# Optimization experiments

Measured on AMD Instinct MI355X. Metric: run time of the kernel, lower is better.

The kernel has to match this reference:

```python
import jax, jax.numpy as jnp
import numpy as np

B, N, H = 32, 1024, 512
THR = 0.05  # peak_detection_threshold


def _l2norm(x):
    return x / jnp.linalg.norm(x, axis=-1, keepdims=True)


def setup_inputs() -> dict:
    key = jax.random.key(0)
    ks = jax.random.split(key, 6)
    def w(k, shape, fan_in):
        return jax.random.normal(k, shape, jnp.float32) / np.float32(np.sqrt(fan_in))
    return {
        "segment_rep": jax.random.normal(ks[0], (B, N, H), jnp.float32),
        "phn_mask": jnp.ones((B, N), jnp.float32),
        # SegmentSimilarityMeasure: Linear(2H->H), ReLU, Linear(H->1, no bias)
        "W1": w(ks[1], (2 * H, H), 2 * H),
        "b1": jnp.zeros((H,), jnp.float32),
        "W2": w(ks[2], (H, 1), H),
        # word_enc: Linear(H->H), ReLU, Linear(H->H)
        "We1": w(ks[3], (H, H), H),
        "be1": jnp.zeros((H,), jnp.float32),
        "We2": w(ks[4], (H, H), H),
        "be2": jnp.zeros((H,), jnp.float32),
    }


def _forward(segment_rep, phn_mask, W1, b1, W2, We1, be1, We2, be2):
    Bs, Np, Hd = segment_rep.shape
    # adjacent segment similarity: MLP on concat of l2-normalized neighbors -> (B, N-1)
    cat = jnp.concatenate([_l2norm(segment_rep[:, :-1, :]), _l2norm(segment_rep[:, 1:, :])], axis=2)
    S = (jax.nn.relu(cat @ W1 + b1) @ W2)[..., 0]

    # relative dissimilarity
    Smin = jnp.min(S, axis=1, keepdims=True)
    Smax = jnp.max(S, axis=1, keepdims=True)
    D = 1.0 - (S - Smin) / (Smax - Smin)

    # peak detector (faithful to original, incl. final overwrite of first-order cols -2:)
    z = jnp.zeros_like(D)
    fo = z
    fo = fo.at[:, 0].set(jnp.maximum(D[:, 0] - D[:, 1], 0.0))
    fo = fo.at[:, 1:-1].set(jnp.minimum(jnp.maximum(D[:, 1:-1] - D[:, :-2], 0.0),
                                        jnp.maximum(D[:, 1:-1] - D[:, 2:], 0.0)))
    fo = fo.at[:, -1].set(jnp.maximum(D[:, -1] - D[:, -2], 0.0))
    so = z
    so = so.at[:, 0:2].set(jnp.maximum(D[:, 0:2] - D[:, 2:4], 0.0))
    so = so.at[:, 2:-2].set(jnp.minimum(jnp.maximum(D[:, 2:-2] - D[:, :-4], 0.0),
                                        jnp.maximum(D[:, 2:-2] - D[:, 4:], 0.0)))
    fo = fo.at[:, -2:].set(jnp.maximum(D[:, -2:] - D[:, -4:-2], 0.0))  # replicates original code
    P = jnp.minimum(jnp.maximum(jnp.maximum(fo, so) - THR, 0.0), fo)

    # pad, mask, straight-through hard boundaries
    P = jnp.pad(P, ((0, 0), (0, 1)))
    P = jax.nn.relu(P + (phn_mask - 1.0))
    b_soft = jnp.tanh(10.0 * P)
    b_hard = jnp.tanh(100000.0 * P)
    b = b_soft + jax.lax.stop_gradient(b_hard - b_soft)
    b = jnp.cumsum(b, axis=1)  # (B, N)
    b = b + (b[:, :1] == 0).astype(b.dtype)  # per-row +1 if b[:,0]==0
    num_word_segments = b[:, -1].astype(jnp.int32) + 1  # (B,)

    # U: column j holds j+1 for j < num_word_segments[i], else -100000. Nmax = N (static bound).
    cols = jnp.arange(1, Np + 1, dtype=jnp.int32)  # (Nmax,)
    U = jnp.where(cols[None, :] <= num_word_segments[:, None],
                  cols.astype(segment_rep.dtype)[None, :], -100000.0)  # (B, Nmax)

    V = U[:, None, :] - b[:, :, None]  # (B, N, Nmax)
    Wseg = 1.0 - jnp.tanh(100000.0 * jnp.abs(V))
    Wseg = Wseg / jnp.sum(Wseg, axis=1, keepdims=True)
    Wseg = jnp.nan_to_num(Wseg)

    # pool: (B, Nmax, N) @ (B, N, H) -> (B, Nmax, H)
    word_rep = jnp.einsum('bnm,bnh->bmh', Wseg, segment_rep)
    word_masks = jnp.where(word_rep == 0, 0.0, 1.0)
    out = jax.nn.relu(word_rep @ We1 + be1) @ We2 + be2
    return out * word_masks


def reference(segment_rep, phn_mask, W1, b1, W2, We1, be1, We2, be2):
    return _forward(segment_rep, phn_mask, W1, b1, W2, We1, be1, We2, be2)
```

## Files before the change

### kernel.cpp

```cpp
#include <hip/hip_runtime.h>

#define BB 32
#define NN 1024
#define HH 512
#define NS 1023

typedef unsigned short u16;
typedef unsigned int   u32;
typedef __attribute__((ext_vector_type(8))) short bf16x8;
typedef __attribute__((ext_vector_type(4))) float f32x4;

__device__ __forceinline__ float bf2f(u16 h) {
  union { u32 u; float f; } c; c.u = ((u32)h) << 16; return c.f;
}
__device__ __forceinline__ u16 f2bf(float f) {
  union { float f; u32 u; } c; c.f = f;
  u32 u = c.u;
  return (u16)((u + 0x7fffu + ((u >> 16) & 1u)) >> 16);
}
__device__ __forceinline__ void split_bf(float x, u16& hi, u16& lo) {
  hi = f2bf(x);
  lo = f2bf(x - bf2f(hi));
}
__device__ __forceinline__ void dma16(const u16* g, u16* l) {
  __builtin_amdgcn_global_load_lds(
      (const __attribute__((address_space(1))) u32*)g,
      (__attribute__((address_space(3))) u32*)l, 16, 0, 0);
}

__global__ __launch_bounds__(256) void k_prep_a(const float* __restrict__ seg,
                                                u16* __restrict__ ahi,
                                                u16* __restrict__ alo) {
  int row = blockIdx.x * 4 + (threadIdx.x >> 6);
  int lane = threadIdx.x & 63;
  const float4* p = (const float4*)(seg + ((size_t)row << 9) + lane * 8);
  float4 a = p[0], b = p[1];
  float v[8] = {a.x, a.y, a.z, a.w, b.x, b.y, b.z, b.w};
  float s = 0.f;
#pragma unroll
  for (int i = 0; i < 8; ++i) s += v[i] * v[i];
#pragma unroll
  for (int m = 32; m; m >>= 1) s += __shfl_xor(s, m, 64);
  float nrm = sqrtf(s);
  u16 h[8], l[8];
#pragma unroll
  for (int i = 0; i < 8; ++i) split_bf(v[i] / nrm, h[i], l[i]);
  size_t off = ((size_t)row << 9) + lane * 8;
  *(uint4*)(ahi + off) = make_uint4(h[0] | (h[1] << 16), h[2] | (h[3] << 16),
                                    h[4] | (h[5] << 16), h[6] | (h[7] << 16));
  *(uint4*)(alo + off) = make_uint4(l[0] | (l[1] << 16), l[2] | (l[3] << 16),
                                    l[4] | (l[5] << 16), l[6] | (l[7] << 16));
}

__global__ __launch_bounds__(256) void k_tr3(const float* __restrict__ W1,
                                             const float* __restrict__ We1,
                                             const float* __restrict__ We2,
                                             u16* __restrict__ w1h,
                                             u16* __restrict__ w1l,
                                             u16* __restrict__ we1t,
                                             u16* __restrict__ we2t) {
  __shared__ u16 Th[64 * 66], Tl[64 * 66];
  int z = blockIdx.z;
  const float* src; u16 *dh, *dl; int K, N;
  if (z == 0)      { src = W1;  dh = w1h;  dl = w1l;          K = 1024; N = 512; }
  else if (z == 1) { src = We1; dh = we1t; dl = (u16*)0;      K = 512;  N = 512; }
  else             { src = We2; dh = we2t; dl = (u16*)0;      K = 512;  N = 512; }
  if (blockIdx.y * 64 >= K) return;
  int nb = blockIdx.x * 64, kb = blockIdx.y * 64;
  int tid = threadIdx.x;
#pragma unroll
  for (int i = 0; i < 16; ++i) {
    int e = tid + i * 256;
    int r = e >> 6, c = e & 63;
    float v = src[(size_t)(kb + r) * N + nb + c];
    u16 hi, lo; split_bf(v, hi, lo);
    Th[c * 66 + r] = hi;
    Tl[c * 66 + r] = lo;
  }
  __syncthreads();
#pragma unroll
  for (int i = 0; i < 16; ++i) {
    int e = tid + i * 256;
    int n = e >> 6, k = e & 63;
    dh[(size_t)(nb + n) * K + kb + k] = Th[n * 66 + k];
    if (dl) dl[(size_t)(nb + n) * K + kb + k] = Tl[n * 66 + k];
  }
}

__global__ __launch_bounds__(512, 2) void k_sgemm(const u16* __restrict__ ahi,
                                                  const u16* __restrict__ alo,
                                                  const u16* __restrict__ w1h,
                                                  const u16* __restrict__ w1l,
                                                  const float* __restrict__ b1,
                                                  const float* __restrict__ W2,
                                                  float* __restrict__ Spart) {
  __shared__ u16 Ah[2][256 * 32];
  __shared__ u16 Al[2][256 * 32];
  __shared__ u16 Bh[2][256 * 32];
  __shared__ u16 Bl[2][256 * 32];

  const int tid  = threadIdx.x;
  const int wave = tid >> 6, lane = tid & 63;
  const int quad = lane >> 4, l15 = lane & 15;
  const int wm = wave >> 2, wn = wave & 3;
  const int r_in = lane >> 2, c_in = lane & 3;
  const int w    = blockIdx.x;
  const int xcd  = w & 7, slot = w >> 3;
  const int nblk = slot & 1;
  const int mblk = xcd * 16 + (slot >> 1);
  const int mrow0 = mblk * 256;
  const int ncol0 = nblk * 256;

#define SG_AH(tb_, ks_)                                                      \
  {                                                                          \
    int k0_ = (ks_) * 32, half_ = k0_ >> 9, cb_ = k0_ & 511;                 \
    int g0_ = mrow0 + wave * 32 + r_in + half_;                              \
    int g1_ = g0_ + 16;                                                      \
    if (g0_ > 32767) g0_ = 32767;                                            \
    if (g1_ > 32767) g1_ = 32767;                                            \
    dma16(ahi + ((((size_t)g0_) << 9) + cb_ + c_in * 8),                     \
          &Ah[tb_][(wave * 32) * 32]);                                       \
    dma16(ahi + ((((size_t)g1_) << 9) + cb_ + c_in * 8),                     \
          &Ah[tb_][(wave * 32 + 16) * 32]);                                  \
  }
#define SG_AL(tb_, ks_)                                                      \
  {                                                                          \
    int k0_ = (ks_) * 32, half_ = k0_ >> 9, cb_ = k0_ & 511;                 \
    int g0_ = mrow0 + wave * 32 + r_in + half_;                              \
    int g1_ = g0_ + 16;                                                      \
    if (g0_ > 32767) g0_ = 32767;                                            \
    if (g1_ > 32767) g1_ = 32767;                                            \
    dma16(alo + ((((size_t)g0_) << 9) + cb_ + c_in * 8),                     \
          &Al[tb_][(wave * 32) * 32]);                                       \
    dma16(alo + ((((size_t)g1_) << 9) + cb_ + c_in * 8),                     \
          &Al[tb_][(wave * 32 + 16) * 32]);                                  \
  }
#define SG_BH(tb_, ks_)                                                      \
  {                                                                          \
    int k0_ = (ks_) * 32;                                                    \
    int n0_ = ncol0 + wave * 32 + r_in;                                      \
    dma16(w1h + (((size_t)n0_) << 10) + k0_ + c_in * 8,                      \
          &Bh[tb_][(wave * 32) * 32]);                                       \
    dma16(w1h + (((size_t)(n0_ + 16)) << 10) + k0_ + c_in * 8,               \
          &Bh[tb_][(wave * 32 + 16) * 32]);                                  \
  }
#define SG_BL(tb_, ks_)                                                      \
  {                                                                          \
    int k0_ = (ks_) * 32;                                                    \
    int n0_ = ncol0 + wave * 32 + r_in;                                      \
    dma16(w1l + (((size_t)n0_) << 10) + k0_ + c_in * 8,                      \
          &Bl[tb_][(wave * 32) * 32]);                                       \
    dma16(w1l + (((size_t)(n0_ + 16)) << 10) + k0_ + c_in * 8,               \
          &Bl[tb_][(wave * 32 + 16) * 32]);                                  \
  }

  f32x4 acc[8][4];
#pragma unroll
  for (int mi = 0; mi < 8; ++mi)
#pragma unroll
    for (int ni = 0; ni < 4; ++ni) acc[mi][ni] = (f32x4){0.f, 0.f, 0.f, 0.f};

  SG_AH(0, 0) SG_BH(0, 0) SG_BL(0, 0) SG_AL(0, 0)
  __syncthreads();

  for (int ks = 0; ks < 32; ++ks) {
    const int bb = ks & 1;
    const int nx = (ks + 1 < 32) ? ks + 1 : 31;

    SG_AH(bb ^ 1, nx) SG_BH(bb ^ 1, nx) SG_BL(bb ^ 1, nx) SG_AL(bb ^ 1, nx)

    bf16x8 ah[8], al[8], bh[4], bl[4];
#pragma unroll
    for (int mi = 0; mi < 8; ++mi)
      ah[mi] = *(const bf16x8*)&Ah[bb][(wm * 128 + mi * 16 + l15) * 32 + quad * 8];
#pragma unroll
    for (int ni = 0; ni < 4; ++ni)
      bh[ni] = *(const bf16x8*)&Bh[bb][(wn * 64 + ni * 16 + l15) * 32 + quad * 8];
    __builtin_amdgcn_s_setprio(1);
#pragma unroll
    for (int ni = 0; ni < 4; ++ni)
#pragma unroll
      for (int mi = 0; mi < 8; ++mi)
        acc[mi][ni] = __builtin_amdgcn_mfma_f32_16x16x32_bf16(ah[mi], bh[ni], acc[mi][ni], 0, 0, 0);
#pragma unroll
    for (int ni = 0; ni < 4; ++ni)
      bl[ni] = *(const bf16x8*)&Bl[bb][(wn * 64 + ni * 16 + l15) * 32 + quad * 8];
#pragma unroll
    for (int ni = 0; ni < 4; ++ni)
#pragma unroll
      for (int mi = 0; mi < 8; ++mi)
        acc[mi][ni] = __builtin_amdgcn_mfma_f32_16x16x32_bf16(ah[mi], bl[ni], acc[mi][ni], 0, 0, 0);
#pragma unroll
    for (int mi = 0; mi < 8; ++mi)
      al[mi] = *(const bf16x8*)&Al[bb][(wm * 128 + mi * 16 + l15) * 32 + quad * 8];
#pragma unroll
    for (int ni = 0; ni < 4; ++ni)
#pragma unroll
      for (int mi = 0; mi < 8; ++mi)
        acc[mi][ni] = __builtin_amdgcn_mfma_f32_16x16x32_bf16(al[mi], bh[ni], acc[mi][ni], 0, 0, 0);
    __builtin_amdgcn_s_setprio(0);

    __syncthreads();
  }
#undef SG_AH
#undef SG_AL
#undef SG_BH
#undef SG_BL

  float* red = (float*)&Ah[0][0];
  float b1v[4], w2v[4];
#pragma unroll
  for (int ni = 0; ni < 4; ++ni) {
    int n_g = ncol0 + wn * 64 + ni * 16 + l15;
    b1v[ni] = b1[n_g];
    w2v[ni] = W2[n_g];
  }
#pragma unroll
  for (int mi = 0; mi < 8; ++mi) {
#pragma unroll
    for (int reg = 0; reg < 4; ++reg) {
      float part = 0.f;
#pragma unroll
      for (int ni = 0; ni < 4; ++ni) {
        float h = acc[mi][ni][reg] + b1v[ni];
        h = h > 0.f ? h : 0.f;
        part = fmaf(h, w2v[ni], part);
      }
#pragma unroll
      for (int m = 8; m; m >>= 1) part += __shfl_xor(part, m, 64);
      if (l15 == 0) red[wave * 128 + mi * 16 + quad * 4 + reg] = part;
    }
  }
  __syncthreads();
  if (tid < 256) {
    int wmr = tid >> 7, rl = tid & 127;
    float s = red[(wmr * 4 + 0) * 128 + rl] + red[(wmr * 4 + 1) * 128 + rl]
            + red[(wmr * 4 + 2) * 128 + rl] + red[(wmr * 4 + 3) * 128 + rl];
    int grow = mrow0 + tid;
    int b = grow >> 10, n = grow & 1023;
    if (n < NS)
      Spart[((size_t)nblk * BB + b) * NN + n] = s;
  }
}

__global__ __launch_bounds__(256) void k_row(const float* __restrict__ S0,
                                             const float* __restrict__ S1,
                                             const float* __restrict__ mask,
                                             int* __restrict__ assign,
                                             float* __restrict__ weight,
                                             float* __restrict__ total,
                                             int* __restrict__ startn,
                                             int* __restrict__ endn) {
  int b = blockIdx.x, tid = threadIdx.x;
  __shared__ float Ssh[NS];
  __shared__ float Dsh[NS];
  __shared__ float tsh[NN];
  __shared__ float bsh[NN];
  __shared__ float totl[NN];
  __shared__ int   stl[NN];
  __shared__ int   enl[NN];
  __shared__ float red[256];

  for (int n = tid; n < NS; n += 256)
    Ssh[n] = S0[((size_t)b << 10) + n] + S1[((size_t)b << 10) + n];
  __syncthreads();

  float mn = INFINITY, mx = -INFINITY;
  for (int n = tid; n < NS; n += 256) {
    float v = Ssh[n];
    mn = fminf(mn, v); mx = fmaxf(mx, v);
  }
  red[tid] = mn; __syncthreads();
  for (int s = 128; s; s >>= 1) { if (tid < s) red[tid] = fminf(red[tid], red[tid + s]); __syncthreads(); }
  float Smin = red[0]; __syncthreads();
  red[tid] = mx; __syncthreads();
  for (int s = 128; s; s >>= 1) { if (tid < s) red[tid] = fmaxf(red[tid], red[tid + s]); __syncthreads(); }
  float Smax = red[0]; __syncthreads();

  for (int n = tid; n < NS; n += 256)
    Dsh[n] = 1.0f - (Ssh[n] - Smin) / (Smax - Smin);
  __syncthreads();

  for (int n = tid; n < NN; n += 256) {
    float P;
    if (n >= NS) {
      P = 0.f;
    } else {
      float D = Dsh[n];
      float fo, so;
      if (n == 0)            fo = fmaxf(D - Dsh[1], 0.f);
      else if (n >= NS - 2)  fo = fmaxf(D - Dsh[n - 2], 0.f);
      else                   fo = fminf(fmaxf(D - Dsh[n - 1], 0.f),
                                        fmaxf(D - Dsh[n + 1], 0.f));
      if (n <= 1)            so = fmaxf(D - Dsh[n + 2], 0.f);
      else if (n >= NS - 2)  so = 0.f;
      else                   so = fminf(fmaxf(D - Dsh[n - 2], 0.f),
                                        fmaxf(D - Dsh[n + 2], 0.f));
      P = fminf(fmaxf(fmaxf(fo, so) - 0.05f, 0.f), fo);
    }
    float m = mask[((size_t)b << 10) + n];
    P = P + (m - 1.0f);
    P = P > 0.f ? P : 0.f;
    float bs = tanhf(10.0f * P);
    float bh = tanhf(100000.0f * P);
    tsh[n] = bs + (bh - bs);
  }
  __syncthreads();

  if (tid == 0) {
    float acc = 0.f;
    for (int n = 0; n < NN; n += 8) {
      float t0 = tsh[n + 0], t1 = tsh[n + 1], t2 = tsh[n + 2], t3 = tsh[n + 3];
      float t4 = tsh[n + 4], t5 = tsh[n + 5], t6 = tsh[n + 6], t7 = tsh[n + 7];
      acc += t0; bsh[n + 0] = acc; acc += t1; bsh[n + 1] = acc;
      acc += t2; bsh[n + 2] = acc; acc += t3; bsh[n + 3] = acc;
      acc += t4; bsh[n + 4] = acc; acc += t5; bsh[n + 5] = acc;
      acc += t6; bsh[n + 6] = acc; acc += t7; bsh[n + 7] = acc;
    }
  }
  __syncthreads();

  float add1 = (bsh[0] == 0.0f) ? 1.0f : 0.0f;
  int   num  = (int)(bsh[NN - 1] + add1) + 1;

  for (int mi = tid; mi < NN; mi += 256) { totl[mi] = 0.f; stl[mi] = 1 << 30; enl[mi] = -1; }
  __syncthreads();

  for (int n = tid; n < NN; n += 256) {
    float bv = bsh[n] + add1;
    float kf = rintf(bv);
    int   k  = (int)kf;
    int   a  = -1; float w = 0.f;
    if (k >= 1 && k <= num && k <= NN) {
      float v = fabsf(kf - bv);
      w = 1.0f - tanhf(100000.0f * v);
      if (w > 0.f) {
        a = k - 1;
        atomicAdd(&totl[a], w);
        atomicMin(&stl[a], n);
        atomicMax(&enl[a], n);
      } else {
        a = -1; w = 0.f;
      }
    }
    assign[((size_t)b << 10) + n] = a;
    weight[((size_t)b << 10) + n] = w;
  }
  __syncthreads();
  for (int mi = tid; mi < NN; mi += 256) {
    total [((size_t)b << 10) + mi] = totl[mi];
    startn[((size_t)b << 10) + mi] = stl[mi];
    endn  [((size_t)b << 10) + mi] = enl[mi];
  }
}

__global__ __launch_bounds__(64) void k_pool(const float* __restrict__ seg,
                                             const int* __restrict__ assign,
                                             const float* __restrict__ weight,
                                             const float* __restrict__ total,
                                             const int* __restrict__ startn,
                                             const int* __restrict__ endn,
                                             u16* hrep,
                                             unsigned char* __restrict__ mb) {
  int bm = blockIdx.x;
  int b  = bm >> 10, m = bm & 1023;
  int lane = threadIdx.x;
  float acc[8] = {0.f, 0.f, 0.f, 0.f, 0.f, 0.f, 0.f, 0.f};
  float tm = total[bm];
  if (tm > 0.f) {
    int s = startn[bm], e = endn[bm];
    for (int n = s; n <= e; ++n) {
      if (assign[((size_t)b << 10) + n] != m) continue;
      float coef = weight[((size_t)b << 10) + n] / tm;
      const float4* p = (const float4*)(seg + (((size_t)b << 10) + n) * HH + lane * 8);
      float4 x = p[0], y = p[1];
      acc[0] = fmaf(coef, x.x, acc[0]); acc[1] = fmaf(coef, x.y, acc[1]);
      acc[2] = fmaf(coef, x.z, acc[2]); acc[3] = fmaf(coef, x.w, acc[3]);
      acc[4] = fmaf(coef, y.x, acc[4]); acc[5] = fmaf(coef, y.y, acc[5]);
      acc[6] = fmaf(coef, y.z, acc[6]); acc[7] = fmaf(coef, y.w, acc[7]);
    }
  }
  u16 h[8];
  unsigned int mbyte = 0;
#pragma unroll
  for (int j = 0; j < 8; ++j) {
    h[j] = f2bf(acc[j]);
    mbyte |= (acc[j] == 0.f ? 1u : 0u) << j;
  }
  *(uint4*)(hrep + ((size_t)bm << 10) + lane * 8) =
      make_uint4(h[0] | (h[1] << 16), h[2] | (h[3] << 16),
                 h[4] | (h[5] << 16), h[6] | (h[7] << 16));
  mb[((size_t)bm << 6) + lane] = (unsigned char)mbyte;
}

__global__ __launch_bounds__(512, 4) void k_g(const u16* asrc,
                                              const u16* __restrict__ bmat,
                                              const float* __restrict__ bias,
                                              const unsigned char* __restrict__ mb,
                                              float* outp,
                                              u16* hid,
                                              int a_off, int mode) {
  __shared__ u16 As[3][64 * 32];
  __shared__ u16 Bs[2][512 * 32];

  const int tid  = threadIdx.x;
  const int wave = tid >> 6, lane = tid & 63;
  const int quad = lane >> 4, l15 = lane & 15;
  const int wm = wave >> 2, wn = wave & 3;
  const int r_in = lane >> 2, c_in = lane & 3;
  const int mrow0 = blockIdx.x * 64;

#define SGB(tb_, ks_)                                                        \
  {                                                                          \
    int k0_ = (ks_) * 32;                                                    \
    _Pragma("unroll")                                                        \
    for (int g_ = 0; g_ < 4; ++g_) {                                         \
      int n_ = wave * 64 + g_ * 16 + r_in;                                   \
      dma16(bmat + (size_t)n_ * 512 + k0_ + c_in * 8,                        \
            &Bs[tb_][(wave * 64 + g_ * 16) * 32]);                           \
    }                                                                        \
  }
#define SGA(sl_, ks_)                                                        \
  {                                                                          \
    if (wave < 4) {                                                          \
      int k0_ = (ks_) * 32;                                                  \
      int row_ = wave * 16 + r_in;                                           \
      dma16(asrc + ((size_t)(mrow0 + row_) << 10) + a_off + k0_ + c_in * 8,  \
            &As[sl_][(wave * 16) * 32]);                                     \
    }                                                                        \
  }

  f32x4 acc[2][8];
#pragma unroll
  for (int mi = 0; mi < 2; ++mi)
#pragma unroll
    for (int ni = 0; ni < 8; ++ni) acc[mi][ni] = (f32x4){0.f, 0.f, 0.f, 0.f};

  SGB(0, 0) SGA(0, 0) SGA(1, 1)
  if (wave < 4) { asm volatile("s_waitcnt vmcnt(1)" ::: "memory"); }
  else          { asm volatile("s_waitcnt vmcnt(0)" ::: "memory"); }
  __builtin_amdgcn_s_barrier();

  for (int ks = 0; ks < 16; ++ks) {
    const int bb = ks & 1;
    const int ra = ks % 3;
    const int nb = (ks + 1 < 16) ? ks + 1 : 15;
    const int na = (ks + 2 < 16) ? ks + 2 : 15;
    SGB(bb ^ 1, nb)
    SGA((ks + 2) % 3, na)
    bf16x8 a[2], b[8];
#pragma unroll
    for (int mi = 0; mi < 2; ++mi)
      a[mi] = *(const bf16x8*)&As[ra][(wm * 32 + mi * 16 + l15) * 32 + quad * 8];
#pragma unroll
    for (int ni = 0; ni < 8; ++ni)
      b[ni] = *(const bf16x8*)&Bs[bb][(wn * 128 + ni * 16 + l15) * 32 + quad * 8];
    asm volatile("s_waitcnt lgkmcnt(0)" ::: "memory");
    __builtin_amdgcn_sched_barrier(0);
    __builtin_amdgcn_s_setprio(1);
#pragma unroll
    for (int ni = 0; ni < 8; ++ni)
#pragma unroll
      for (int mi = 0; mi < 2; ++mi)
        acc[mi][ni] = __builtin_amdgcn_mfma_f32_16x16x32_bf16(a[mi], b[ni], acc[mi][ni], 0, 0, 0);
    __builtin_amdgcn_s_setprio(0);
    if (wave < 4) { asm volatile("s_waitcnt vmcnt(1)" ::: "memory"); }
    else          { asm volatile("s_waitcnt vmcnt(0)" ::: "memory"); }
    __builtin_amdgcn_s_barrier();
  }
#undef SGB
#undef SGA
  asm volatile("s_waitcnt vmcnt(0)" ::: "memory");

  float bv[8];
#pragma unroll
  for (int ni = 0; ni < 8; ++ni) bv[ni] = bias[wn * 128 + ni * 16 + l15];

  if (mode == 1) {
#pragma unroll
    for (int mi = 0; mi < 2; ++mi)
#pragma unroll
      for (int ni = 0; ni < 8; ++ni)
#pragma unroll
        for (int reg = 0; reg < 4; ++reg) {
          int col = wn * 128 + ni * 16 + l15;
          int row = mrow0 + wm * 32 + mi * 16 + quad * 4 + reg;
          float h = acc[mi][ni][reg] + bv[ni];
          h = h > 0.f ? h : 0.f;
          hid[((size_t)row << 10) + 512 + col] = f2bf(h);
        }
  } else {
#pragma unroll
    for (int mi = 0; mi < 2; ++mi)
#pragma unroll
      for (int ni = 0; ni < 8; ++ni)
#pragma unroll
        for (int reg = 0; reg < 4; ++reg) {
          int col = wn * 128 + ni * 16 + l15;
          int row = mrow0 + wm * 32 + mi * 16 + quad * 4 + reg;
          float o = acc[mi][ni][reg] + bv[ni];
          unsigned char m8 = mb[((size_t)row << 6) + (col >> 3)];
          outp[((size_t)row << 9) + col] = ((m8 >> (col & 7)) & 1) ? 0.f : o;
        }
  }
}

__global__ void k_diag(float* __restrict__ out, int hostcode) {
  if (hostcode != 0) out[0] = (float)hostcode;
}

extern "C" void kernel_launch(void* const* d_in, const int* in_sizes, int n_in,
                              void* d_out, int out_size, void* d_ws, size_t ws_size,
                              hipStream_t stream) {
  const float* seg  = (const float*)d_in[0];
  const float* mask = (const float*)d_in[1];
  const float* W1   = (const float*)d_in[2];
  const float* b1   = (const float*)d_in[3];
  const float* W2   = (const float*)d_in[4];
  const float* We1  = (const float*)d_in[5];
  const float* be1  = (const float*)d_in[6];
  const float* We2  = (const float*)d_in[7];
  const float* be2  = (const float*)d_in[8];

  const size_t NROW = (size_t)BB * NN;
  float* ws = (float*)d_ws;
  float* S0     = ws;
  float* S1     = S0 + NROW;
  int*   assign = (int*)(S1 + NROW);
  float* weight = (float*)(assign + NROW);
  float* total  = weight + NROW;
  int*   startn = (int*)(total + NROW);
  int*   endn   = startn + NROW;
  u16*   w1h    = (u16*)(endn + NROW);
  u16*   w1l    = w1h + (size_t)512 * 1024;
  u16*   we1t   = w1l + (size_t)512 * 1024;
  u16*   we2t   = we1t + (size_t)512 * 512;

  float* out = (float*)d_out;
  u16*   ahi = (u16*)d_out;
  u16*   alo = ahi + (size_t)NROW * HH;
  u16*   hrep = (u16*)d_out;
  unsigned char* mbuf = (unsigned char*)w1h;

  int hostcode = 0;
  if (ws_size < (size_t)7 * NROW * 4 + (size_t)3 * 1024 * 1024) hostcode += 32768;
  if (out_size != 16777216) hostcode += 8192;

  k_prep_a<<<dim3(BB * NN / 4), dim3(256), 0, stream>>>(seg, ahi, alo);
  k_tr3   <<<dim3(8, 16, 3), dim3(256), 0, stream>>>(W1, We1, We2, w1h, w1l, we1t, we2t);
  k_sgemm <<<dim3(256), dim3(512), 0, stream>>>(ahi, alo, w1h, w1l, b1, W2, S0);
  k_row   <<<dim3(BB), dim3(256), 0, stream>>>(S0, S1, mask, assign, weight, total, startn, endn);
  k_pool  <<<dim3(BB * NN), dim3(64), 0, stream>>>(seg, assign, weight, total, startn, endn, hrep, mbuf);
  k_g     <<<dim3(512), dim3(512), 0, stream>>>(hrep, we1t, be1, mbuf, out, hrep, 0,   1);
  k_g     <<<dim3(512), dim3(512), 0, stream>>>(hrep, we2t, be2, mbuf, out, hrep, 512, 2);
  k_diag  <<<dim3(1), dim3(1), 0, stream>>>(out, hostcode);
}
```

Measured before the change: 319.4 us.

## Software-pipeline split-bf16 GEMM main loop with staged DMA and fine-grained waits

Restructures the W1 GEMM K-loop into three MFMA phases per step, each followed by issuing the next tile's global-to-LDS copies for one operand pair and prefetching that phase's LDS fragments. Full __syncthreads is replaced with explicit vmcnt/lgkmcnt waits plus raw s_barrier, and the next tile's high-part registers are loaded at the end of the prior step using ping-pong register sets. The aim is to overlap LDS reads and global DMA with MFMA execution and to avoid waiting on all outstanding loads at each step. In exchange it raises register pressure, and the hand-picked vmcnt counts have to match the exact DMA issue order for correctness.

```diff
diff --git a/kernel.cpp b/kernel.cpp
--- a/kernel.cpp
+++ b/kernel.cpp
@@ -160,52 +160,90 @@
 #pragma unroll
     for (int ni = 0; ni < 4; ++ni) acc[mi][ni] = (f32x4){0.f, 0.f, 0.f, 0.f};
 
+  const int a_off0 = (wm * 128 + l15) * 32 + quad * 8;
+  const int b_off0 = (wn * 64 + l15) * 32 + quad * 8;
+
+  bf16x8 ahA[8], bhA[4], ahB[8], bhB[4];
+
   SG_AH(0, 0) SG_BH(0, 0) SG_BL(0, 0) SG_AL(0, 0)
-  __syncthreads();
-
-  for (int ks = 0; ks < 32; ++ks) {
-    const int bb = ks & 1;
-    const int nx = (ks + 1 < 32) ? ks + 1 : 31;
-
-    SG_AH(bb ^ 1, nx) SG_BH(bb ^ 1, nx) SG_BL(bb ^ 1, nx) SG_AL(bb ^ 1, nx)
-
-    bf16x8 ah[8], al[8], bh[4], bl[4];
-#pragma unroll
-    for (int mi = 0; mi < 8; ++mi)
-      ah[mi] = *(const bf16x8*)&Ah[bb][(wm * 128 + mi * 16 + l15) * 32 + quad * 8];
-#pragma unroll
-    for (int ni = 0; ni < 4; ++ni)
-      bh[ni] = *(const bf16x8*)&Bh[bb][(wn * 64 + ni * 16 + l15) * 32 + quad * 8];
-    __builtin_amdgcn_s_setprio(1);
-#pragma unroll
-    for (int ni = 0; ni < 4; ++ni)
-#pragma unroll
-      for (int mi = 0; mi < 8; ++mi)
-        acc[mi][ni] = __builtin_amdgcn_mfma_f32_16x16x32_bf16(ah[mi], bh[ni], acc[mi][ni], 0, 0, 0);
-#pragma unroll
-    for (int ni = 0; ni < 4; ++ni)
-      bl[ni] = *(const bf16x8*)&Bl[bb][(wn * 64 + ni * 16 + l15) * 32 + quad * 8];
-#pragma unroll
-    for (int ni = 0; ni < 4; ++ni)
-#pragma unroll
-      for (int mi = 0; mi < 8; ++mi)
-        acc[mi][ni] = __builtin_amdgcn_mfma_f32_16x16x32_bf16(ah[mi], bl[ni], acc[mi][ni], 0, 0, 0);
-#pragma unroll
-    for (int mi = 0; mi < 8; ++mi)
-      al[mi] = *(const bf16x8*)&Al[bb][(wm * 128 + mi * 16 + l15) * 32 + quad * 8];
-#pragma unroll
-    for (int ni = 0; ni < 4; ++ni)
-#pragma unroll
-      for (int mi = 0; mi < 8; ++mi)
-        acc[mi][ni] = __builtin_amdgcn_mfma_f32_16x16x32_bf16(al[mi], bh[ni], acc[mi][ni], 0, 0, 0);
-    __builtin_amdgcn_s_setprio(0);
-
-    __syncthreads();
-  }
+  asm volatile("s_waitcnt vmcnt(2)" ::: "memory");
+  __builtin_amdgcn_s_barrier();
+#pragma unroll
+  for (int mi = 0; mi < 8; ++mi) ahA[mi] = *(const bf16x8*)&Ah[0][a_off0 + mi * 512];
+#pragma unroll
+  for (int ni = 0; ni < 4; ++ni) bhA[ni] = *(const bf16x8*)&Bh[0][b_off0 + ni * 512];
+
+#define STEP(bb_, ks_, AH_IN, BH_IN, AH_OUT, BH_OUT)                         \
+  {                                                                          \
+    const int nx_ = ((ks_) + 1 < 32) ? ((ks_) + 1) : 31;                     \
+    bf16x8 bl_[4], al_[8];                                                   \
+                     \
+    asm volatile("s_waitcnt lgkmcnt(0)" ::: "memory");                       \
+    __builtin_amdgcn_sched_barrier(0);                                       \
+    __builtin_amdgcn_s_setprio(1);                                           \
+    _Pragma("unroll")                                                        \
+    for (int ni_ = 0; ni_ < 4; ++ni_)                                        \
+      _Pragma("unroll")                                                      \
+      for (int mi_ = 0; mi_ < 8; ++mi_)                                      \
+        acc[mi_][ni_] = __builtin_amdgcn_mfma_f32_16x16x32_bf16(             \
+            AH_IN[mi_], BH_IN[ni_], acc[mi_][ni_], 0, 0, 0);                 \
+    __builtin_amdgcn_s_setprio(0);                                           \
+    SG_AH((bb_) ^ 1, nx_) SG_BH((bb_) ^ 1, nx_)                              \
+    _Pragma("unroll")                                                        \
+    for (int ni_ = 0; ni_ < 4; ++ni_)                                        \
+      bl_[ni_] = *(const bf16x8*)&Bl[bb_][b_off0 + ni_ * 512];               \
+    asm volatile("s_waitcnt vmcnt(4)" ::: "memory");                         \
+    __builtin_amdgcn_s_barrier();                                            \
+                     \
+    asm volatile("s_waitcnt lgkmcnt(0)" ::: "memory");                       \
+    __builtin_amdgcn_sched_barrier(0);                                       \
+    __builtin_amdgcn_s_setprio(1);                                           \
+    _Pragma("unroll")                                                        \
+    for (int ni_ = 0; ni_ < 4; ++ni_)                                        \
+      _Pragma("unroll")                                                      \
+      for (int mi_ = 0; mi_ < 8; ++mi_)                                      \
+        acc[mi_][ni_] = __builtin_amdgcn_mfma_f32_16x16x32_bf16(             \
+            AH_IN[mi_], bl_[ni_], acc[mi_][ni_], 0, 0, 0);                   \
+    __builtin_amdgcn_s_setprio(0);                                           \
+    SG_BL((bb_) ^ 1, nx_) SG_AL((bb_) ^ 1, nx_)                              \
+    _Pragma("unroll")                                                        \
+    for (int mi_ = 0; mi_ < 8; ++mi_)                                        \
+      al_[mi_] = *(const bf16x8*)&Al[bb_][a_off0 + mi_ * 512];               \
+    asm volatile("s_waitcnt vmcnt(4)" ::: "memory");                         \
+    __builtin_amdgcn_s_barrier();                                            \
+                              \
+    asm volatile("s_waitcnt lgkmcnt(0)" ::: "memory");                       \
+    __builtin_amdgcn_sched_barrier(0);                                       \
+    __builtin_amdgcn_s_setprio(1);                                           \
+    _Pragma("unroll")                                                        \
+    for (int ni_ = 0; ni_ < 4; ++ni_)                                        \
+      _Pragma("unroll")                                                      \
+      for (int mi_ = 0; mi_ < 8; ++mi_)                                      \
+        acc[mi_][ni_] = __builtin_amdgcn_mfma_f32_16x16x32_bf16(             \
+            al_[mi_], BH_IN[ni_], acc[mi_][ni_], 0, 0, 0);                   \
+    __builtin_amdgcn_s_setprio(0);                                           \
+    _Pragma("unroll")                                                        \
+    for (int mi_ = 0; mi_ < 8; ++mi_)                                        \
+      AH_OUT[mi_] = *(const bf16x8*)&Ah[(bb_) ^ 1][a_off0 + mi_ * 512];      \
+    _Pragma("unroll")                                                        \
+    for (int ni_ = 0; ni_ < 4; ++ni_)                                        \
+      BH_OUT[ni_] = *(const bf16x8*)&Bh[(bb_) ^ 1][b_off0 + ni_ * 512];      \
+    asm volatile("s_waitcnt vmcnt(2)" ::: "memory");                         \
+    __builtin_amdgcn_s_barrier();                                            \
+  }
+
+  for (int ks = 0; ks < 32; ks += 2) {
+    STEP(0, ks,     ahA, bhA, ahB, bhB)
+    STEP(1, ks + 1, ahB, bhB, ahA, bhA)
+  }
+#undef STEP
 #undef SG_AH
 #undef SG_AL
 #undef SG_BH
 #undef SG_BL
+
+  asm volatile("s_waitcnt vmcnt(0)" ::: "memory");
+  __syncthreads();
 
   float* red = (float*)&Ah[0][0];
   float b1v[4], w2v[4];
```

Result: no change. 319.9 us (+0.2%).
